# Kernel tuning notes

Measured on AMD Instinct MI355X. Metric: run time of the kernel, lower is better.

The kernel has to match this reference:

```python
import jax, jax.numpy as jnp
import numpy as np

L2_REG_STRENGTH = 0.001  # l2_reg_strength from init


def setup_inputs() -> dict:
    key = jax.random.key(0)
    k1, k2, k3 = jax.random.split(key, 3)
    N, D, O = 200000, 64, 8
    X = jax.random.normal(k1, (N, D), dtype=jnp.float32)
    # dags: float mask-like tensor (o, p, c); values in [0,1) as soft adjacency
    dags = jax.random.uniform(k2, (O, D, D), dtype=jnp.float32)
    # learned parameter W: (num_structures, d, d)
    W = jax.random.normal(k3, (O, D, D), dtype=jnp.float32)
    return {"X": X, "dags": dags, "W": W}


def reference(X, dags, W):
    # Original math:
    #   Z = einsum('opc,np->oncp', dags, X)          (huge O,N,C,P intermediate)
    #   x1 = einsum('oncp,opc->onc', Z, W)
    # Fused equivalent: x1[o,n,c] = sum_p X[n,p] * dags[o,p,c] * W[o,p,c]
    WM = dags * W                                    # (O, P, C) masked weights
    x1 = jnp.einsum('np,opc->onc', X, WM)            # batched GEMM, (O, N, C)
    reg = L2_REG_STRENGTH * jnp.sum(W * W, axis=(-2, -1))  # (O,)
    return (x1, dags, reg)
```

## Files before the change

### kernel.cpp

```cpp
#include <hip/hip_runtime.h>


typedef short short8 __attribute__((ext_vector_type(8)));
typedef float f32x4 __attribute__((ext_vector_type(4)));

#define NROWS    200000
#define DAGS_OFF 102400000
#define REG_OFF  102432768
#define O_STRIDE 12800000

__device__ __forceinline__ unsigned short f2bf(float f) {
    union { float f; unsigned int i; } v; v.f = f;
    unsigned int x = v.i;
    unsigned int r = (x + 0x7fffu + ((x >> 16) & 1u)) >> 16;
    return (unsigned short)r;
}

__global__ __launch_bounds__(256) void prep_kernel(
    const float* __restrict__ dags,
    const float* __restrict__ W,
    unsigned short* __restrict__ wmt,
    float* __restrict__ out)
{
    const int o = blockIdx.x;
    const int t = threadIdx.x;
    const float* dg = dags + o * 4096;
    const float* w  = W    + o * 4096;
    unsigned short* wt = wmt + o * 4096;
    float* outd = out + DAGS_OFF + o * 4096;

    float s = 0.f;
    #pragma unroll
    for (int i = 0; i < 16; ++i) {
        int e = i * 256 + t;
        int p = e >> 6, c = e & 63;
        float dv = dg[e];
        float wv = w[e];
        wt[c * 64 + p] = f2bf(dv * wv);
        outd[e] = dv;
        s += wv * wv;
    }
    #pragma unroll
    for (int off = 32; off > 0; off >>= 1) s += __shfl_down(s, off);
    __shared__ float red[4];
    if ((t & 63) == 0) red[t >> 6] = s;
    __syncthreads();
    if (t == 0) {
        out[REG_OFF + o] = 0.001f * (red[0] + red[1] + red[2] + red[3]);
    }
}

__global__ __launch_bounds__(256, 4) void gemm_kernel(
    const float* __restrict__ X,
    const unsigned short* __restrict__ wmt,
    float* __restrict__ out)
{
    const int t    = threadIdx.x;
    const int w    = t >> 6;
    const int lane = t & 63;
    const int r    = lane & 15;
    const int q    = lane >> 4;

    const int nb = blockIdx.x * 64 + w * 16 + r;

    const f32x4 xf0 = *reinterpret_cast<const f32x4*>(X + nb * 64 + q * 8);
    const f32x4 xf1 = *reinterpret_cast<const f32x4*>(X + nb * 64 + q * 8 + 4);
    const f32x4 xf2 = *reinterpret_cast<const f32x4*>(X + nb * 64 + 32 + q * 8);
    const f32x4 xf3 = *reinterpret_cast<const f32x4*>(X + nb * 64 + 32 + q * 8 + 4);
    short8 xk0, xk1;
    #pragma unroll
    for (int j = 0; j < 4; ++j) {
        xk0[j]     = (short)f2bf(xf0[j]);
        xk0[4 + j] = (short)f2bf(xf1[j]);
        xk1[j]     = (short)f2bf(xf2[j]);
        xk1[4 + j] = (short)f2bf(xf3[j]);
    }

    #pragma unroll
    for (int o = 0; o < 8; ++o) {
        const unsigned short* wp = wmt + o * 4096;
        float* outp = out + o * O_STRIDE + nb * 64;
        #pragma unroll
        for (int ct = 0; ct < 4; ++ct) {
            const int c = ct * 16 + r;
            short8 a0 = *reinterpret_cast<const short8*>(wp + c * 64 + q * 8);
            short8 a1 = *reinterpret_cast<const short8*>(wp + c * 64 + 32 + q * 8);
            f32x4 acc = {0.f, 0.f, 0.f, 0.f};
            acc = __builtin_amdgcn_mfma_f32_16x16x32_bf16(a0, xk0, acc, 0, 0, 0);
            acc = __builtin_amdgcn_mfma_f32_16x16x32_bf16(a1, xk1, acc, 0, 0, 0);
            *reinterpret_cast<f32x4*>(outp + ct * 16 + q * 4) = acc;
        }
    }
}

extern "C" void kernel_launch(void* const* d_in, const int* in_sizes, int n_in,
                              void* d_out, int out_size, void* d_ws, size_t ws_size,
                              hipStream_t stream)
{
    const float* X    = (const float*)d_in[0];
    const float* dags = (const float*)d_in[1];
    const float* W    = (const float*)d_in[2];
    float* out = (float*)d_out;
    unsigned short* wmt = (unsigned short*)d_ws;

    prep_kernel<<<8, 256, 0, stream>>>(dags, W, wmt, out);
    gemm_kernel<<<NROWS / 64, 256, 0, stream>>>(X, wmt, out);
}
```

Baseline: 507.2 us.

## Assign one output structure per wave and keep its weights in registers

The GEMM kernel is restructured so each of 8 waves in a 512-thread block owns one structure o and loads its masked-weight fragments into registers once. Each block then loops over 160 rows in 5 tiles of 32. This removes the repeated per-row weight reloads from the old layout, where every wave walked all 8 structures. The cost is that each of the 8 waves now loads and converts the same X rows on its own, and the grid has fewer, larger blocks.

```diff
diff --git a/kernel.cpp b/kernel.cpp
--- a/kernel.cpp
+++ b/kernel.cpp
@@ -8,6 +8,9 @@
 #define DAGS_OFF 102400000
 #define REG_OFF  102432768
 #define O_STRIDE 12800000
+
+#define ROWS_PER_BLOCK 160
+#define GRID_GEMM      1250
 
 __device__ __forceinline__ unsigned short f2bf(float f) {
     union { float f; unsigned int i; } v; v.f = f;
@@ -50,45 +53,56 @@
     }
 }
 
-__global__ __launch_bounds__(256, 4) void gemm_kernel(
+__global__ __launch_bounds__(512) void gemm_kernel(
     const float* __restrict__ X,
     const unsigned short* __restrict__ wmt,
     float* __restrict__ out)
 {
     const int t    = threadIdx.x;
-    const int w    = t >> 6;
+    const int o    = t >> 6;
     const int lane = t & 63;
     const int r    = lane & 15;
     const int q    = lane >> 4;
 
-    const int nb = blockIdx.x * 64 + w * 16 + r;
-
-    const f32x4 xf0 = *reinterpret_cast<const f32x4*>(X + nb * 64 + q * 8);
-    const f32x4 xf1 = *reinterpret_cast<const f32x4*>(X + nb * 64 + q * 8 + 4);
-    const f32x4 xf2 = *reinterpret_cast<const f32x4*>(X + nb * 64 + 32 + q * 8);
-    const f32x4 xf3 = *reinterpret_cast<const f32x4*>(X + nb * 64 + 32 + q * 8 + 4);
-    short8 xk0, xk1;
+    const unsigned short* wp = wmt + o * 4096;
+    short8 a[4][2];
     #pragma unroll
-    for (int j = 0; j < 4; ++j) {
-        xk0[j]     = (short)f2bf(xf0[j]);
-        xk0[4 + j] = (short)f2bf(xf1[j]);
-        xk1[j]     = (short)f2bf(xf2[j]);
-        xk1[4 + j] = (short)f2bf(xf3[j]);
+    for (int ct = 0; ct < 4; ++ct) {
+        a[ct][0] = *reinterpret_cast<const short8*>(wp + (ct * 16 + r) * 64 + q * 8);
+        a[ct][1] = *reinterpret_cast<const short8*>(wp + (ct * 16 + r) * 64 + 32 + q * 8);
     }
 
+    const int rowbase = blockIdx.x * ROWS_PER_BLOCK;
+    float* const outo = out + o * O_STRIDE;
+
     #pragma unroll
-    for (int o = 0; o < 8; ++o) {
-        const unsigned short* wp = wmt + o * 4096;
-        float* outp = out + o * O_STRIDE + nb * 64;
+    for (int tile = 0; tile < 5; ++tile) {
         #pragma unroll
-        for (int ct = 0; ct < 4; ++ct) {
-            const int c = ct * 16 + r;
-            short8 a0 = *reinterpret_cast<const short8*>(wp + c * 64 + q * 8);
-            short8 a1 = *reinterpret_cast<const short8*>(wp + c * 64 + 32 + q * 8);
-            f32x4 acc = {0.f, 0.f, 0.f, 0.f};
-            acc = __builtin_amdgcn_mfma_f32_16x16x32_bf16(a0, xk0, acc, 0, 0, 0);
-            acc = __builtin_amdgcn_mfma_f32_16x16x32_bf16(a1, xk1, acc, 0, 0, 0);
-            *reinterpret_cast<f32x4*>(outp + ct * 16 + q * 4) = acc;
+        for (int s = 0; s < 2; ++s) {
+            const int nb = rowbase + tile * 32 + s * 16 + r;
+            const float* xp = X + nb * 64;
+
+            const f32x4 xf0 = *reinterpret_cast<const f32x4*>(xp + q * 8);
+            const f32x4 xf1 = *reinterpret_cast<const f32x4*>(xp + q * 8 + 4);
+            const f32x4 xf2 = *reinterpret_cast<const f32x4*>(xp + 32 + q * 8);
+            const f32x4 xf3 = *reinterpret_cast<const f32x4*>(xp + 32 + q * 8 + 4);
+            short8 xk0, xk1;
+            #pragma unroll
+            for (int j = 0; j < 4; ++j) {
+                xk0[j]     = (short)f2bf(xf0[j]);
+                xk0[4 + j] = (short)f2bf(xf1[j]);
+                xk1[j]     = (short)f2bf(xf2[j]);
+                xk1[4 + j] = (short)f2bf(xf3[j]);
+            }
+
+            float* outp = outo + nb * 64;
+            #pragma unroll
+            for (int ct = 0; ct < 4; ++ct) {
+                f32x4 acc = {0.f, 0.f, 0.f, 0.f};
+                acc = __builtin_amdgcn_mfma_f32_16x16x32_bf16(a[ct][0], xk0, acc, 0, 0, 0);
+                acc = __builtin_amdgcn_mfma_f32_16x16x32_bf16(a[ct][1], xk1, acc, 0, 0, 0);
+                *reinterpret_cast<f32x4*>(outp + ct * 16 + q * 4) = acc;
+            }
         }
     }
 }
@@ -104,5 +118,5 @@
     unsigned short* wmt = (unsigned short*)d_ws;
 
     prep_kernel<<<8, 256, 0, stream>>>(dags, W, wmt, out);
-    gemm_kernel<<<NROWS / 64, 256, 0, stream>>>(X, wmt, out);
+    gemm_kernel<<<GRID_GEMM, 512, 0, stream>>>(X, wmt, out);
 }
```

After: 499.7 us. Within noise of the previous version (-1.5%).
